# Optimization experiments

Measured on AMD Instinct MI355X. Metric: run time of the kernel, lower is better.

## Reference

```python
import jax, jax.numpy as jnp
import numpy as np
from jax import lax

Q = 8          # num quantization bins (co_matrix_shape[0])
K = 3          # spatial filter size (spatial_shape = [K,K,K])
PAD = (K - 1) // 2


def setup_inputs() -> dict:
    key = jax.random.key(0)
    k1, k2, k3 = jax.random.split(key, 3)
    # uniform [0,1) so floor((x-min)/max * Q) stays in [0, Q-1] (matches valid torch index_select)
    x = jax.random.uniform(k1, (8, 16, 256, 256), dtype=jnp.float32)
    co_matrix = jax.random.normal(k2, (Q, Q), dtype=jnp.float32)
    spatial_filter = jax.random.normal(k3, (K, K, K), dtype=jnp.float32)
    return {"input": x, "co_matrix": co_matrix, "spatial_filter": spatial_filter}


def _quantize(x, num_q):
    # faithful to the torch code: norm = (x - min) / max  (NOT max-min)
    x_min = jnp.min(x)
    x_max = jnp.max(x)
    idx = jnp.floor((x - x_min) / x_max * num_q).astype(jnp.int32)  # [N,c,h,w]
    return idx


def reference(input, co_matrix, spatial_filter):
    x = input
    N, c, h, w = x.shape
    idx = _quantize(x, Q)                                  # [N,c,h,w] int32

    # Vectorize the per-bin loop: gather row i of co_matrix at every pixel's bin index.
    # cof[i] = co_matrix[i, idx]  -> [Q,N,c,h,w]
    cof = co_matrix[:, idx]
    conv_in = (cof * x[None]).reshape(Q * N, 1, c, h, w)   # [Q*N,1,c,h,w]

    w3d = spatial_filter.reshape(1, 1, K, K, K)
    spatial = lax.conv_general_dilated(
        conv_in, w3d,
        window_strides=(1, 1, 1),
        padding=[(PAD, PAD)] * 3,
        dimension_numbers=("NCDHW", "OIDHW", "NCDHW"),
    ).reshape(Q, N, c, h, w)

    # torch code convolves the mask with a 1x1x1 ones filter at stride 1 -> identity
    mask = (idx[None] == jnp.arange(Q, dtype=jnp.int32)[:, None, None, None, None])
    conv_out = jnp.sum(mask.astype(x.dtype) * spatial, axis=0)  # [N,c,h,w]
    return (conv_out, co_matrix, spatial_filter, idx)
```

## Files before the change

kernel.cpp:

```cpp
#include <hip/hip_runtime.h>
#include <stdint.h>

typedef __fp16 h2 __attribute__((ext_vector_type(2)));

__device__ uint32_t g_slots[512];
__device__ __align__(16) uint32_t g_tbl[32];

__device__ __forceinline__ uint32_t mapf(float f) {
  uint32_t u = __float_as_uint(f);
  return (u & 0x80000000u) ? ~u : (u | 0x80000000u);
}
__device__ __forceinline__ float unmapf(uint32_t m) {
  return (m & 0x80000000u) ? __uint_as_float(m & 0x7FFFFFFFu) : __uint_as_float(~m);
}

__device__ __forceinline__ float fdot2f(h2 a, h2 b, float c) {
#if __has_builtin(__builtin_amdgcn_fdot2)
  return __builtin_amdgcn_fdot2(a, b, c, false);
#else
  float d;
  asm("v_dot2_f32_f16 %0, %1, %2, %3" : "=v"(d) : "v"(a), "v"(b), "v"(c));
  return d;
#endif
}

__global__ __launch_bounds__(256) void k_minmax(const float* __restrict__ x, int n4, int ntail,
                                                const float* __restrict__ co, const float* __restrict__ sfil,
                                                float* __restrict__ out_co, float* __restrict__ out_sf) {
  __shared__ float smn[256], smx[256];
  int tid = threadIdx.x;
  float mn = 3.0e38f, mx = -3.0e38f;
  const float4* x4 = (const float4*)x;
  int stride = gridDim.x * blockDim.x;
  #pragma unroll 4
  for (int i = blockIdx.x * blockDim.x + tid; i < n4; i += stride) {
    float4 v = x4[i];
    mn = fminf(mn, fminf(fminf(v.x, v.y), fminf(v.z, v.w)));
    mx = fmaxf(mx, fmaxf(fmaxf(v.x, v.y), fmaxf(v.z, v.w)));
  }
  if (blockIdx.x == 0 && tid == 0) {
    for (int i = 4 * n4; i < 4 * n4 + ntail; ++i) { mn = fminf(mn, x[i]); mx = fmaxf(mx, x[i]); }
  }
  smn[tid] = mn; smx[tid] = mx;
  __syncthreads();
  for (int s = 128; s > 0; s >>= 1) {
    if (tid < s) { smn[tid] = fminf(smn[tid], smn[tid + s]); smx[tid] = fmaxf(smx[tid], smx[tid + s]); }
    __syncthreads();
  }
  if (tid == 0) {
    int slot = (blockIdx.x & 15) * 16;
    atomicMax(&g_slots[slot], mapf(smx[0]));
    atomicMax(&g_slots[256 + slot], mapf(-smn[0]));
  }
  if (blockIdx.x == 0) {
    if (tid < 8) {
      const float* r = co + tid * 8;
      float rmn = r[0], rmx = r[0];
      #pragma unroll
      for (int j = 1; j < 8; ++j) { rmn = fminf(rmn, r[j]); rmx = fmaxf(rmx, r[j]); }
      float rs = (rmx - rmn) * (1.0f / 255.0f);
      if (rs < 1e-30f) rs = 1.0f;
      uint32_t d0 = 0, d1 = 0;
      #pragma unroll
      for (int j = 0; j < 8; ++j) {
        int b = (int)lrintf((r[j] - rmn) / rs);
        b = b < 0 ? 0 : (b > 255 ? 255 : b);
        if (j < 4) d0 |= ((uint32_t)b) << (8 * j);
        else       d1 |= ((uint32_t)b) << (8 * (j - 4));
      }
      g_tbl[4 * tid + 0] = d0;
      g_tbl[4 * tid + 1] = d1;
      g_tbl[4 * tid + 2] = __float_as_uint(rs);
      g_tbl[4 * tid + 3] = __float_as_uint(rmn);
    }
    if (tid < 64) out_co[tid] = co[tid];
    if (tid < 27) out_sf[tid] = sfil[tid];
  }
}

__device__ __forceinline__ float quant_d8(float xv, float mn, float mx8, float y8) {
  float s   = xv - mn;
  float t08 = s * y8;
  float r0  = __builtin_fmaf(-mx8, t08, s);
  return __builtin_fmaf(r0, y8, t08);
}

__global__ __launch_bounds__(256, 8) void k_conv(const float* __restrict__ x, const float* __restrict__ sfil,
                                              float* __restrict__ out, float* __restrict__ out_idx) {
  __shared__ __align__(16) uint32_t xsu[2640];
  __shared__ __align__(16) uint32_t qls[1320];
  __shared__ __align__(16) uint4    tbl[8];
  __shared__ uint32_t anyw[4];

  int tid = threadIdx.x;
  int b = blockIdx.x;
  int wt = b & 1, ht = (b >> 1) & 31, ct = (b >> 6) & 7, n = b >> 9;
  int c0 = ct * 2, h0 = ht * 8, w0 = wt * 128;
  int nbase = n * 16;

  if (tid < 8) tbl[tid] = ((const uint4*)g_tbl)[tid];

  uint32_t ma = 0u, mb = 0u;
  #pragma unroll
  for (int i = 0; i < 16; ++i) {
    uint32_t a = g_slots[i * 16], bq = g_slots[256 + i * 16];
    ma = ma > a ? ma : a;
    mb = mb > bq ? mb : bq;
  }
  float mx = unmapf(ma);
  float mn = -unmapf(mb);
  float y   = 1.0f / mx;
  float y8  = y * 8.0f;
  float mx8 = mx * 0.125f;

  const int tx = tid & 31, ty = tid >> 5;
  int qmaxv = 0;

  {
    #pragma unroll
    for (int it = 0; it < 5; ++it) {
      int rr = ty + 8 * it;
      int lc = (rr * 13) >> 7;
      int lh = rr - 10 * lc;
      int c = c0 - 1 + lc, h = h0 - 1 + lh;
      bool chok = ((unsigned)c < 16u) & ((unsigned)h < 256u);
      int chbase = ((nbase + c) << 16) + (h << 8);
      int wq = w0 + 4 * tx;
      float4 vb = float4{0.f, 0.f, 0.f, 0.f};
      if (chok) vb = *(const float4*)&x[chbase + wq];
      float pe = __shfl_up(vb.w, 1);
      if (tx == 0) {
        int wm = wq - 1;
        pe = (chok & (wm >= 0)) ? x[chbase + wm] : 0.0f;
      }
      float xv[4] = {pe, vb.x, vb.y, vb.z};
      uint32_t qu[4];
      #pragma unroll
      for (int j = 0; j < 4; ++j) {
        int q = (int)quant_d8(xv[j], mn, mx8, y8);
        qmaxv = max(qmaxv, q);
        qu[j] = min((uint32_t)q, 7u);
      }
      uint32_t b01 = __builtin_amdgcn_perm(qu[1], qu[0], 0x0c0c0400u);
      uint32_t b23 = __builtin_amdgcn_perm(qu[3], qu[2], 0x04000c0cu);
      h2 lo = __builtin_amdgcn_cvt_pkrtz(xv[0], xv[1]);
      h2 hi = __builtin_amdgcn_cvt_pkrtz(xv[2], xv[3]);
      uint2 wv; wv.x = __builtin_bit_cast(uint32_t, lo); wv.y = __builtin_bit_cast(uint32_t, hi);
      *(uint2*)&xsu[rr * 66 + 2 * tx] = wv;
      qls[rr * 33 + tx] = b01 | b23;
    }
    if (tid < 40) {
      int rr = tid;
      int lc = (rr * 13) >> 7;
      int lh = rr - 10 * lc;
      int c = c0 - 1 + lc, h = h0 - 1 + lh;
      bool chok = ((unsigned)c < 16u) & ((unsigned)h < 256u);
      int chbase = ((nbase + c) << 16) + (h << 8);
      int wq = w0 + 128;
      float4 vb = float4{0.f, 0.f, 0.f, 0.f};
      if (chok & (wq < 256)) vb = *(const float4*)&x[chbase + wq];
      float pe = chok ? x[chbase + wq - 1] : 0.0f;
      float xv[4] = {pe, vb.x, vb.y, vb.z};
      uint32_t qu[4];
      #pragma unroll
      for (int j = 0; j < 4; ++j) {
        int q = (int)quant_d8(xv[j], mn, mx8, y8);
        qmaxv = max(qmaxv, q);
        qu[j] = min((uint32_t)q, 7u);
      }
      uint32_t b01 = __builtin_amdgcn_perm(qu[1], qu[0], 0x0c0c0400u);
      uint32_t b23 = __builtin_amdgcn_perm(qu[3], qu[2], 0x04000c0cu);
      h2 lo = __builtin_amdgcn_cvt_pkrtz(xv[0], xv[1]);
      h2 hi = __builtin_amdgcn_cvt_pkrtz(xv[2], xv[3]);
      uint2 wv; wv.x = __builtin_bit_cast(uint32_t, lo); wv.y = __builtin_bit_cast(uint32_t, hi);
      *(uint2*)&xsu[rr * 66 + 64] = wv;
      qls[rr * 33 + 32] = b01 | b23;
    }
  }
  anyw[tid >> 6] = (uint32_t)__any(qmaxv > 7);
  __syncthreads();
  uint32_t any8 = anyw[0] | anyw[1] | anyw[2] | anyw[3];

  uint32_t wAs[9], wBs[9];
  #pragma unroll
  for (int r = 0; r < 9; ++r) {
    h2 a  = __builtin_amdgcn_cvt_pkrtz(sfil[3 * r], sfil[3 * r + 1]);
    h2 bq = __builtin_amdgcn_cvt_pkrtz(sfil[3 * r + 2], 0.0f);
    wAs[r] = (uint32_t)__builtin_amdgcn_readfirstlane((int)__builtin_bit_cast(uint32_t, a));
    wBs[r] = (uint32_t)__builtin_amdgcn_readfirstlane((int)__builtin_bit_cast(uint32_t, bq));
  }

  const h2 one2 = {(__fp16)1.0f, (__fp16)1.0f};
  const uint32_t SELK[4] = {0x03020100u, 0x04030201u, 0x05040302u, 0x06050403u};
  const int tw = tx, th = ty;

  for (int c = 0; c < 2; ++c) {
    int qbase = (c * 10 + th) * 33 + tw;
    int xbase = (c * 10 + th) * 66 + 2 * tw;

    int qc = qbase + 11 * 33;
    uint32_t Qc0 = qls[qc], Qc1 = qls[qc + 1];
    uint32_t q4 = __builtin_amdgcn_perm(Qc1, Qc0, 0x04030201u);
    uint32_t rlo[4], rhi[4]; float rs4[4], rcp4[4];
    #pragma unroll
    for (int k = 0; k < 4; ++k) {
      uint32_t qk = (q4 >> (8 * k)) & 0xffu;
      uint4 T = tbl[qk];
      rlo[k] = T.x; rhi[k] = T.y;
      rs4[k] = __uint_as_float(T.z);
      rcp4[k] = __builtin_fmaf(-1024.0f, rs4[k], __uint_as_float(T.w));
    }

    float acc1[4] = {0.f, 0.f, 0.f, 0.f};
    float acc2[4] = {0.f, 0.f, 0.f, 0.f};
    #pragma unroll
    for (int dc = 0; dc < 3; ++dc) {
      #pragma unroll
      for (int di = 0; di < 3; ++di) {
        int xo = xbase + (dc * 10 + di) * 66;
        int qo = qbase + (dc * 10 + di) * 33;
        uint2 px = *(const uint2*)&xsu[xo];
        uint32_t p2u = xsu[xo + 2];
        uint32_t Q0 = qls[qo], Q1 = qls[qo + 1];
        uint32_t m01 = __builtin_amdgcn_alignbit(px.y, px.x, 16);
        uint32_t m12 = __builtin_amdgcn_alignbit(p2u, px.y, 16);
        uint32_t xAu[4] = {px.x, m01, px.y, m12};
        uint32_t xBu[3] = {px.y, m12, p2u};
        int r = dc * 3 + di;
        h2 wA = __builtin_bit_cast(h2, wAs[r]);
        h2 wB = __builtin_bit_cast(h2, wBs[r]);
        h2 wB2 = __builtin_bit_cast(h2, wBs[r] << 16);
        #pragma unroll
        for (int k = 0; k < 4; ++k) {
          uint32_t sel = __builtin_amdgcn_perm(Q1, Q0, SELK[k]);
          uint32_t bb  = __builtin_amdgcn_perm(rhi[k], rlo[k], sel);
          uint32_t fA  = __builtin_amdgcn_perm(0x64646464u, bb, 0x04010400u);
          h2 pA = wA * __builtin_bit_cast(h2, xAu[k]);
          acc1[k] = fdot2f(pA, __builtin_bit_cast(h2, fA), acc1[k]);
          acc2[k] = fdot2f(pA, one2, acc2[k]);
          h2 pB; uint32_t fB;
          if (k < 3) {
            fB = __builtin_amdgcn_perm(0x64646464u, bb, 0x04040402u);
            pB = wB * __builtin_bit_cast(h2, xBu[k]);
          } else {
            fB = __builtin_amdgcn_perm(0x64646464u, bb, 0x04020404u);
            pB = wB2 * __builtin_bit_cast(h2, p2u);
          }
          acc1[k] = fdot2f(pB, __builtin_bit_cast(h2, fB), acc1[k]);
          acc2[k] = fdot2f(pB, one2, acc2[k]);
        }
      }
    }

    int gbase = ((nbase + c0 + c) << 16) + ((h0 + th) << 8) + (w0 + 4 * tw);
    float idxf[4], vals[4];
    if (!any8) {
      #pragma unroll
      for (int k = 0; k < 4; ++k) {
        idxf[k] = (float)((q4 >> (8 * k)) & 0xffu);
        vals[k] = __builtin_fmaf(rs4[k], acc1[k], rcp4[k] * acc2[k]);
      }
    } else {
      float4 cxv = *(const float4*)&x[gbase];
      float cx[4] = {cxv.x, cxv.y, cxv.z, cxv.w};
      #pragma unroll
      for (int k = 0; k < 4; ++k) {
        float d8 = quant_d8(cx[k], mn, mx8, y8);
        idxf[k] = truncf(d8);
        float v = __builtin_fmaf(rs4[k], acc1[k], rcp4[k] * acc2[k]);
        vals[k] = (d8 >= 8.0f) ? 0.0f : v;
      }
    }

    *(float4*)&out[gbase] = float4{vals[0], vals[1], vals[2], vals[3]};
    out_idx[gbase + 0] = idxf[0];
    *(float2*)&out_idx[gbase + 1] = float2{idxf[1], idxf[2]};
    out_idx[gbase + 3] = idxf[3];
  }
}

extern "C" void kernel_launch(void* const* d_in, const int* in_sizes, int n_in,
                              void* d_out, int out_size, void* d_ws, size_t ws_size,
                              hipStream_t stream) {
  const float* x    = (const float*)d_in[0];
  const float* co   = (const float*)d_in[1];
  const float* sfil = (const float*)d_in[2];
  float* out = (float*)d_out;
  int nx = in_sizes[0];

  int n4 = nx / 4, ntail = nx - 4 * n4;

  float* out_co  = out + nx;
  float* out_sf  = out + nx + 64;
  float* out_idx = out + nx + 64 + 27;

  k_minmax<<<512, 256, 0, stream>>>(x, n4, ntail, co, sfil, out_co, out_sf);
  k_conv<<<4096, 256, 0, stream>>>(x, sfil, out, out_idx);
}
```

Measured before the change: 124.5 us.

## Fuse min/max reduction and conv into one cooperative kernel with grid sync

Merges the global min/max reduction and the quantized 3D conv into a single cooperative kernel. A grid-wide barrier separates the two phases, and each block then processes two conv tiles. Each block builds the co-matrix table in shared memory itself instead of reading it from a global buffer. This removes a kernel launch and the gap between launches, at the cost of a grid sync and a residency requirement of 2048 blocks. If the cooperative launch fails, the code falls back to the two-kernel path.

Result: slower. 362.8 us (+191.5%).

```diff
diff --git a/kernel.cpp b/kernel.cpp
--- a/kernel.cpp
+++ b/kernel.cpp
@@ -1,5 +1,8 @@
 #include <hip/hip_runtime.h>
+#include <hip/hip_cooperative_groups.h>
 #include <stdint.h>
+
+namespace cg = cooperative_groups;
 
 typedef __fp16 h2 __attribute__((ext_vector_type(2)));
 
@@ -22,6 +25,267 @@
   asm("v_dot2_f32_f16 %0, %1, %2, %3" : "=v"(d) : "v"(a), "v"(b), "v"(c));
   return d;
 #endif
+}
+
+__device__ __forceinline__ float quant_d8(float xv, float mn, float mx8, float y8) {
+  float s   = xv - mn;
+  float t08 = s * y8;
+  float r0  = __builtin_fmaf(-mx8, t08, s);
+  return __builtin_fmaf(r0, y8, t08);
+}
+
+__device__ __forceinline__ uint4 build_tbl_row(const float* __restrict__ co, int row) {
+  const float* r = co + row * 8;
+  float rmn = r[0], rmx = r[0];
+  #pragma unroll
+  for (int j = 1; j < 8; ++j) { rmn = fminf(rmn, r[j]); rmx = fmaxf(rmx, r[j]); }
+  float rs = (rmx - rmn) * (1.0f / 255.0f);
+  if (rs < 1e-30f) rs = 1.0f;
+  uint32_t d0 = 0, d1 = 0;
+  #pragma unroll
+  for (int j = 0; j < 8; ++j) {
+    int b = (int)lrintf((r[j] - rmn) / rs);
+    b = b < 0 ? 0 : (b > 255 ? 255 : b);
+    if (j < 4) d0 |= ((uint32_t)b) << (8 * j);
+    else       d1 |= ((uint32_t)b) << (8 * (j - 4));
+  }
+  return uint4{d0, d1, __float_as_uint(rs), __float_as_uint(rmn)};
+}
+
+__global__ __launch_bounds__(256, 8) void k_fused(const float* __restrict__ x, int n4, int ntail,
+                                                  const float* __restrict__ co, const float* __restrict__ sfil,
+                                                  float* __restrict__ out, float* __restrict__ out_idx,
+                                                  float* __restrict__ out_co, float* __restrict__ out_sf) {
+  __shared__ __align__(16) uint32_t xsu[2640];
+  __shared__ __align__(16) uint32_t qls[1320];
+  __shared__ __align__(16) uint4    tbl[8];
+  __shared__ uint32_t anyw[4];
+
+  int tid = threadIdx.x;
+  int bid = blockIdx.x;
+
+  {
+    float* smn = (float*)xsu;
+    float* smx = smn + 256;
+    float mn = 3.0e38f, mx = -3.0e38f;
+    const float4* x4 = (const float4*)x;
+    int stride = gridDim.x * blockDim.x;
+    #pragma unroll 4
+    for (int i = bid * blockDim.x + tid; i < n4; i += stride) {
+      float4 v = x4[i];
+      mn = fminf(mn, fminf(fminf(v.x, v.y), fminf(v.z, v.w)));
+      mx = fmaxf(mx, fmaxf(fmaxf(v.x, v.y), fmaxf(v.z, v.w)));
+    }
+    if (bid == 0 && tid == 0) {
+      for (int i = 4 * n4; i < 4 * n4 + ntail; ++i) { mn = fminf(mn, x[i]); mx = fmaxf(mx, x[i]); }
+    }
+    smn[tid] = mn; smx[tid] = mx;
+    __syncthreads();
+    for (int s = 128; s > 0; s >>= 1) {
+      if (tid < s) { smn[tid] = fminf(smn[tid], smn[tid + s]); smx[tid] = fmaxf(smx[tid], smx[tid + s]); }
+      __syncthreads();
+    }
+    if (tid == 0) {
+      int slot = (bid & 15) * 16;
+      atomicMax(&g_slots[slot], mapf(smx[0]));
+      atomicMax(&g_slots[256 + slot], mapf(-smn[0]));
+    }
+    if (bid == 0) {
+      if (tid < 64) out_co[tid] = co[tid];
+      if (tid < 27) out_sf[tid] = sfil[tid];
+    }
+  }
+  __syncthreads();
+
+  if (tid < 8) tbl[tid] = build_tbl_row(co, tid);
+
+  cg::this_grid().sync();
+
+  uint32_t ma = 0u, mb = 0u;
+  #pragma unroll
+  for (int i = 0; i < 16; ++i) {
+    uint32_t a = g_slots[i * 16], bq = g_slots[256 + i * 16];
+    ma = ma > a ? ma : a;
+    mb = mb > bq ? mb : bq;
+  }
+  float mx = unmapf(ma);
+  float mn = -unmapf(mb);
+  float y   = 1.0f / mx;
+  float y8  = y * 8.0f;
+  float mx8 = mx * 0.125f;
+
+  uint32_t wAs[9], wBs[9];
+  #pragma unroll
+  for (int r = 0; r < 9; ++r) {
+    h2 a  = __builtin_amdgcn_cvt_pkrtz(sfil[3 * r], sfil[3 * r + 1]);
+    h2 bq = __builtin_amdgcn_cvt_pkrtz(sfil[3 * r + 2], 0.0f);
+    wAs[r] = (uint32_t)__builtin_amdgcn_readfirstlane((int)__builtin_bit_cast(uint32_t, a));
+    wBs[r] = (uint32_t)__builtin_amdgcn_readfirstlane((int)__builtin_bit_cast(uint32_t, bq));
+  }
+
+  const h2 one2 = {(__fp16)1.0f, (__fp16)1.0f};
+  const uint32_t SELK[4] = {0x03020100u, 0x04030201u, 0x05040302u, 0x06050403u};
+  const int tx = tid & 31, ty = tid >> 5;
+  const int tw = tx, th = ty;
+
+  for (int tt = 0; tt < 2; ++tt) {
+    int t = 2 * bid + tt;
+    int wt = t & 1, ht = (t >> 1) & 31, ct = (t >> 6) & 7, n = t >> 9;
+    int c0 = ct * 2, h0 = ht * 8, w0 = wt * 128;
+    int nbase = n * 16;
+    int qmaxv = 0;
+
+    __syncthreads();
+
+    {
+      #pragma unroll
+      for (int it = 0; it < 5; ++it) {
+        int rr = ty + 8 * it;
+        int lc = (rr * 13) >> 7;
+        int lh = rr - 10 * lc;
+        int c = c0 - 1 + lc, h = h0 - 1 + lh;
+        bool chok = ((unsigned)c < 16u) & ((unsigned)h < 256u);
+        int chbase = ((nbase + c) << 16) + (h << 8);
+        int wq = w0 + 4 * tx;
+        float4 vb = float4{0.f, 0.f, 0.f, 0.f};
+        if (chok) vb = *(const float4*)&x[chbase + wq];
+        float pe = __shfl_up(vb.w, 1);
+        if (tx == 0) {
+          int wm = wq - 1;
+          pe = (chok & (wm >= 0)) ? x[chbase + wm] : 0.0f;
+        }
+        float xv[4] = {pe, vb.x, vb.y, vb.z};
+        uint32_t qu[4];
+        #pragma unroll
+        for (int j = 0; j < 4; ++j) {
+          int q = (int)quant_d8(xv[j], mn, mx8, y8);
+          qmaxv = max(qmaxv, q);
+          qu[j] = min((uint32_t)q, 7u);
+        }
+        uint32_t b01 = __builtin_amdgcn_perm(qu[1], qu[0], 0x0c0c0400u);
+        uint32_t b23 = __builtin_amdgcn_perm(qu[3], qu[2], 0x04000c0cu);
+        h2 lo = __builtin_amdgcn_cvt_pkrtz(xv[0], xv[1]);
+        h2 hi = __builtin_amdgcn_cvt_pkrtz(xv[2], xv[3]);
+        uint2 wv; wv.x = __builtin_bit_cast(uint32_t, lo); wv.y = __builtin_bit_cast(uint32_t, hi);
+        *(uint2*)&xsu[rr * 66 + 2 * tx] = wv;
+        qls[rr * 33 + tx] = b01 | b23;
+      }
+      if (tid < 40) {
+        int rr = tid;
+        int lc = (rr * 13) >> 7;
+        int lh = rr - 10 * lc;
+        int c = c0 - 1 + lc, h = h0 - 1 + lh;
+        bool chok = ((unsigned)c < 16u) & ((unsigned)h < 256u);
+        int chbase = ((nbase + c) << 16) + (h << 8);
+        int wq = w0 + 128;
+        float4 vb = float4{0.f, 0.f, 0.f, 0.f};
+        if (chok & (wq < 256)) vb = *(const float4*)&x[chbase + wq];
+        float pe = chok ? x[chbase + wq - 1] : 0.0f;
+        float xv[4] = {pe, vb.x, vb.y, vb.z};
+        uint32_t qu[4];
+        #pragma unroll
+        for (int j = 0; j < 4; ++j) {
+          int q = (int)quant_d8(xv[j], mn, mx8, y8);
+          qmaxv = max(qmaxv, q);
+          qu[j] = min((uint32_t)q, 7u);
+        }
+        uint32_t b01 = __builtin_amdgcn_perm(qu[1], qu[0], 0x0c0c0400u);
+        uint32_t b23 = __builtin_amdgcn_perm(qu[3], qu[2], 0x04000c0cu);
+        h2 lo = __builtin_amdgcn_cvt_pkrtz(xv[0], xv[1]);
+        h2 hi = __builtin_amdgcn_cvt_pkrtz(xv[2], xv[3]);
+        uint2 wv; wv.x = __builtin_bit_cast(uint32_t, lo); wv.y = __builtin_bit_cast(uint32_t, hi);
+        *(uint2*)&xsu[rr * 66 + 64] = wv;
+        qls[rr * 33 + 32] = b01 | b23;
+      }
+    }
+    anyw[tid >> 6] = (uint32_t)__any(qmaxv > 7);
+    __syncthreads();
+    uint32_t any8 = anyw[0] | anyw[1] | anyw[2] | anyw[3];
+
+    for (int c = 0; c < 2; ++c) {
+      int qbase = (c * 10 + th) * 33 + tw;
+      int xbase = (c * 10 + th) * 66 + 2 * tw;
+
+      int qc = qbase + 11 * 33;
+      uint32_t Qc0 = qls[qc], Qc1 = qls[qc + 1];
+      uint32_t q4 = __builtin_amdgcn_perm(Qc1, Qc0, 0x04030201u);
+      uint32_t rlo[4], rhi[4]; float rs4[4], rcp4[4];
+      #pragma unroll
+      for (int k = 0; k < 4; ++k) {
+        uint32_t qk = (q4 >> (8 * k)) & 0xffu;
+        uint4 T = tbl[qk];
+        rlo[k] = T.x; rhi[k] = T.y;
+        rs4[k] = __uint_as_float(T.z);
+        rcp4[k] = __builtin_fmaf(-1024.0f, rs4[k], __uint_as_float(T.w));
+      }
+
+      float acc1[4] = {0.f, 0.f, 0.f, 0.f};
+      float acc2[4] = {0.f, 0.f, 0.f, 0.f};
+      #pragma unroll
+      for (int dc = 0; dc < 3; ++dc) {
+        #pragma unroll
+        for (int di = 0; di < 3; ++di) {
+          int xo = xbase + (dc * 10 + di) * 66;
+          int qo = qbase + (dc * 10 + di) * 33;
+          uint2 px = *(const uint2*)&xsu[xo];
+          uint32_t p2u = xsu[xo + 2];
+          uint32_t Q0 = qls[qo], Q1 = qls[qo + 1];
+          uint32_t m01 = __builtin_amdgcn_alignbit(px.y, px.x, 16);
+          uint32_t m12 = __builtin_amdgcn_alignbit(p2u, px.y, 16);
+          uint32_t xAu[4] = {px.x, m01, px.y, m12};
+          uint32_t xBu[3] = {px.y, m12, p2u};
+          int r = dc * 3 + di;
+          h2 wA = __builtin_bit_cast(h2, wAs[r]);
+          h2 wB = __builtin_bit_cast(h2, wBs[r]);
+          h2 wB2 = __builtin_bit_cast(h2, wBs[r] << 16);
+          #pragma unroll
+          for (int k = 0; k < 4; ++k) {
+            uint32_t sel = __builtin_amdgcn_perm(Q1, Q0, SELK[k]);
+            uint32_t bb  = __builtin_amdgcn_perm(rhi[k], rlo[k], sel);
+            uint32_t fA  = __builtin_amdgcn_perm(0x64646464u, bb, 0x04010400u);
+            h2 pA = wA * __builtin_bit_cast(h2, xAu[k]);
+            acc1[k] = fdot2f(pA, __builtin_bit_cast(h2, fA), acc1[k]);
+            acc2[k] = fdot2f(pA, one2, acc2[k]);
+            h2 pB; uint32_t fB;
+            if (k < 3) {
+              fB = __builtin_amdgcn_perm(0x64646464u, bb, 0x04040402u);
+              pB = wB * __builtin_bit_cast(h2, xBu[k]);
+            } else {
+              fB = __builtin_amdgcn_perm(0x64646464u, bb, 0x04020404u);
+              pB = wB2 * __builtin_bit_cast(h2, p2u);
+            }
+            acc1[k] = fdot2f(pB, __builtin_bit_cast(h2, fB), acc1[k]);
+            acc2[k] = fdot2f(pB, one2, acc2[k]);
+          }
+        }
+      }
+
+      int gbase = ((nbase + c0 + c) << 16) + ((h0 + th) << 8) + (w0 + 4 * tw);
+      float idxf[4], vals[4];
+      if (!any8) {
+        #pragma unroll
+        for (int k = 0; k < 4; ++k) {
+          idxf[k] = (float)((q4 >> (8 * k)) & 0xffu);
+          vals[k] = __builtin_fmaf(rs4[k], acc1[k], rcp4[k] * acc2[k]);
+        }
+      } else {
+        float4 cxv = *(const float4*)&x[gbase];
+        float cx[4] = {cxv.x, cxv.y, cxv.z, cxv.w};
+        #pragma unroll
+        for (int k = 0; k < 4; ++k) {
+          float d8 = quant_d8(cx[k], mn, mx8, y8);
+          idxf[k] = truncf(d8);
+          float v = __builtin_fmaf(rs4[k], acc1[k], rcp4[k] * acc2[k]);
+          vals[k] = (d8 >= 8.0f) ? 0.0f : v;
+        }
+      }
+
+      *(float4*)&out[gbase] = float4{vals[0], vals[1], vals[2], vals[3]};
+      out_idx[gbase + 0] = idxf[0];
+      *(float2*)&out_idx[gbase + 1] = float2{idxf[1], idxf[2]};
+      out_idx[gbase + 3] = idxf[3];
+    }
+  }
 }
 
 __global__ __launch_bounds__(256) void k_minmax(const float* __restrict__ x, int n4, int ntail,
@@ -54,35 +318,13 @@
   }
   if (blockIdx.x == 0) {
     if (tid < 8) {
-      const float* r = co + tid * 8;
-      float rmn = r[0], rmx = r[0];
-      #pragma unroll
-      for (int j = 1; j < 8; ++j) { rmn = fminf(rmn, r[j]); rmx = fmaxf(rmx, r[j]); }
-      float rs = (rmx - rmn) * (1.0f / 255.0f);
-      if (rs < 1e-30f) rs = 1.0f;
-      uint32_t d0 = 0, d1 = 0;
-      #pragma unroll
-      for (int j = 0; j < 8; ++j) {
-        int b = (int)lrintf((r[j] - rmn) / rs);
-        b = b < 0 ? 0 : (b > 255 ? 255 : b);
-        if (j < 4) d0 |= ((uint32_t)b) << (8 * j);
-        else       d1 |= ((uint32_t)b) << (8 * (j - 4));
-      }
-      g_tbl[4 * tid + 0] = d0;
-      g_tbl[4 * tid + 1] = d1;
-      g_tbl[4 * tid + 2] = __float_as_uint(rs);
-      g_tbl[4 * tid + 3] = __float_as_uint(rmn);
+      uint4 T = build_tbl_row(co, tid);
+      g_tbl[4 * tid + 0] = T.x; g_tbl[4 * tid + 1] = T.y;
+      g_tbl[4 * tid + 2] = T.z; g_tbl[4 * tid + 3] = T.w;
     }
     if (tid < 64) out_co[tid] = co[tid];
     if (tid < 27) out_sf[tid] = sfil[tid];
   }
-}
-
-__device__ __forceinline__ float quant_d8(float xv, float mn, float mx8, float y8) {
-  float s   = xv - mn;
-  float t08 = s * y8;
-  float r0  = __builtin_fmaf(-mx8, t08, s);
-  return __builtin_fmaf(r0, y8, t08);
 }
 
 __global__ __launch_bounds__(256, 8) void k_conv(const float* __restrict__ x, const float* __restrict__ sfil,
@@ -294,6 +536,12 @@
   float* out_sf  = out + nx + 64;
   float* out_idx = out + nx + 64 + 27;
 
-  k_minmax<<<512, 256, 0, stream>>>(x, n4, ntail, co, sfil, out_co, out_sf);
-  k_conv<<<4096, 256, 0, stream>>>(x, sfil, out, out_idx);
-}
+  void* args[] = {(void*)&x, (void*)&n4, (void*)&ntail, (void*)&co, (void*)&sfil,
+                  (void*)&out, (void*)&out_idx, (void*)&out_co, (void*)&out_sf};
+  hipError_t e = hipLaunchCooperativeKernel((const void*)k_fused, dim3(2048), dim3(256),
+                                            args, 0, stream);
+  if (e != hipSuccess) {
+    k_minmax<<<512, 256, 0, stream>>>(x, n4, ntail, co, sfil, out_co, out_sf);
+    k_conv<<<4096, 256, 0, stream>>>(x, sfil, out, out_idx);
+  }
+}
```

## Share LDS plane loads across two output channels in the 3D stencil loop

Applied to the files above, without the earlier changes.

Restructures the per-thread loop so both output channels are accumulated together. Each input depth plane is loaded from LDS once and reused for every output channel whose 3-tap window covers it, so 12 row loads serve both channels instead of 18. The byte-select perms are also computed once per row rather than once per channel. In exchange it keeps two sets of accumulators and table entries live, which raises register pressure and may lower occupancy.

Result: slower. 205.0 us (+64.7%).

```diff
diff --git a/kernel.cpp b/kernel.cpp
--- a/kernel.cpp
+++ b/kernel.cpp
@@ -194,50 +194,57 @@
   const uint32_t SELK[4] = {0x03020100u, 0x04030201u, 0x05040302u, 0x06050403u};
   const int tw = tx, th = ty;
 
+  uint32_t q4c[2];
+  uint32_t rlo[2][4], rhi[2][4];
+  #pragma unroll
   for (int c = 0; c < 2; ++c) {
-    int qbase = (c * 10 + th) * 33 + tw;
-    int xbase = (c * 10 + th) * 66 + 2 * tw;
-
-    int qc = qbase + 11 * 33;
+    int qc = (c * 10 + th) * 33 + tw + 11 * 33;
     uint32_t Qc0 = qls[qc], Qc1 = qls[qc + 1];
     uint32_t q4 = __builtin_amdgcn_perm(Qc1, Qc0, 0x04030201u);
-    uint32_t rlo[4], rhi[4]; float rs4[4], rcp4[4];
+    q4c[c] = q4;
     #pragma unroll
     for (int k = 0; k < 4; ++k) {
       uint32_t qk = (q4 >> (8 * k)) & 0xffu;
       uint4 T = tbl[qk];
-      rlo[k] = T.x; rhi[k] = T.y;
-      rs4[k] = __uint_as_float(T.z);
-      rcp4[k] = __builtin_fmaf(-1024.0f, rs4[k], __uint_as_float(T.w));
-    }
-
-    float acc1[4] = {0.f, 0.f, 0.f, 0.f};
-    float acc2[4] = {0.f, 0.f, 0.f, 0.f};
+      rlo[c][k] = T.x; rhi[c][k] = T.y;
+    }
+  }
+
+  float acc1[2][4] = {{0.f,0.f,0.f,0.f},{0.f,0.f,0.f,0.f}};
+  float acc2[2][4] = {{0.f,0.f,0.f,0.f},{0.f,0.f,0.f,0.f}};
+
+  #pragma unroll
+  for (int a = 0; a < 4; ++a) {
     #pragma unroll
-    for (int dc = 0; dc < 3; ++dc) {
-      #pragma unroll
-      for (int di = 0; di < 3; ++di) {
-        int xo = xbase + (dc * 10 + di) * 66;
-        int qo = qbase + (dc * 10 + di) * 33;
-        uint2 px = *(const uint2*)&xsu[xo];
-        uint32_t p2u = xsu[xo + 2];
-        uint32_t Q0 = qls[qo], Q1 = qls[qo + 1];
-        uint32_t m01 = __builtin_amdgcn_alignbit(px.y, px.x, 16);
-        uint32_t m12 = __builtin_amdgcn_alignbit(p2u, px.y, 16);
-        uint32_t xAu[4] = {px.x, m01, px.y, m12};
-        uint32_t xBu[3] = {px.y, m12, p2u};
+    for (int di = 0; di < 3; ++di) {
+      int row = a * 10 + th + di;
+      int xo = row * 66 + 2 * tw;
+      int qo = row * 33 + tw;
+      uint2 px = *(const uint2*)&xsu[xo];
+      uint32_t p2u = xsu[xo + 2];
+      uint32_t Q0 = qls[qo], Q1 = qls[qo + 1];
+      uint32_t m01 = __builtin_amdgcn_alignbit(px.y, px.x, 16);
+      uint32_t m12 = __builtin_amdgcn_alignbit(p2u, px.y, 16);
+      uint32_t xAu[4] = {px.x, m01, px.y, m12};
+      uint32_t xBu[3] = {px.y, m12, p2u};
+      uint32_t sel[4];
+      #pragma unroll
+      for (int k = 0; k < 4; ++k) sel[k] = __builtin_amdgcn_perm(Q1, Q0, SELK[k]);
+      #pragma unroll
+      for (int c = 0; c < 2; ++c) {
+        int dc = a - c;
+        if (dc < 0 || dc > 2) continue;
         int r = dc * 3 + di;
         h2 wA = __builtin_bit_cast(h2, wAs[r]);
         h2 wB = __builtin_bit_cast(h2, wBs[r]);
         h2 wB2 = __builtin_bit_cast(h2, wBs[r] << 16);
         #pragma unroll
         for (int k = 0; k < 4; ++k) {
-          uint32_t sel = __builtin_amdgcn_perm(Q1, Q0, SELK[k]);
-          uint32_t bb  = __builtin_amdgcn_perm(rhi[k], rlo[k], sel);
-          uint32_t fA  = __builtin_amdgcn_perm(0x64646464u, bb, 0x04010400u);
+          uint32_t bb = __builtin_amdgcn_perm(rhi[c][k], rlo[c][k], sel[k]);
+          uint32_t fA = __builtin_amdgcn_perm(0x64646464u, bb, 0x04010400u);
           h2 pA = wA * __builtin_bit_cast(h2, xAu[k]);
-          acc1[k] = fdot2f(pA, __builtin_bit_cast(h2, fA), acc1[k]);
-          acc2[k] = fdot2f(pA, one2, acc2[k]);
+          acc1[c][k] = fdot2f(pA, __builtin_bit_cast(h2, fA), acc1[c][k]);
+          acc2[c][k] = fdot2f(pA, one2, acc2[c][k]);
           h2 pB; uint32_t fB;
           if (k < 3) {
             fB = __builtin_amdgcn_perm(0x64646464u, bb, 0x04040402u);
@@ -246,10 +253,23 @@
             fB = __builtin_amdgcn_perm(0x64646464u, bb, 0x04020404u);
             pB = wB2 * __builtin_bit_cast(h2, p2u);
           }
-          acc1[k] = fdot2f(pB, __builtin_bit_cast(h2, fB), acc1[k]);
-          acc2[k] = fdot2f(pB, one2, acc2[k]);
+          acc1[c][k] = fdot2f(pB, __builtin_bit_cast(h2, fB), acc1[c][k]);
+          acc2[c][k] = fdot2f(pB, one2, acc2[c][k]);
         }
       }
+    }
+  }
+
+  #pragma unroll
+  for (int c = 0; c < 2; ++c) {
+    uint32_t q4 = q4c[c];
+    float rs4[4], rcp4[4];
+    #pragma unroll
+    for (int k = 0; k < 4; ++k) {
+      uint32_t qk = (q4 >> (8 * k)) & 0xffu;
+      uint4 T = tbl[qk];
+      rs4[k] = __uint_as_float(T.z);
+      rcp4[k] = __builtin_fmaf(-1024.0f, rs4[k], __uint_as_float(T.w));
     }
 
     int gbase = ((nbase + c0 + c) << 16) + ((h0 + th) << 8) + (w0 + 4 * tw);
@@ -258,7 +278,7 @@
       #pragma unroll
       for (int k = 0; k < 4; ++k) {
         idxf[k] = (float)((q4 >> (8 * k)) & 0xffu);
-        vals[k] = __builtin_fmaf(rs4[k], acc1[k], rcp4[k] * acc2[k]);
+        vals[k] = __builtin_fmaf(rs4[k], acc1[c][k], rcp4[k] * acc2[c][k]);
       }
     } else {
       float4 cxv = *(const float4*)&x[gbase];
@@ -267,7 +287,7 @@
       for (int k = 0; k < 4; ++k) {
         float d8 = quant_d8(cx[k], mn, mx8, y8);
         idxf[k] = truncf(d8);
-        float v = __builtin_fmaf(rs4[k], acc1[k], rcp4[k] * acc2[k]);
+        float v = __builtin_fmaf(rs4[k], acc1[c][k], rcp4[k] * acc2[c][k]);
         vals[k] = (d8 >= 8.0f) ? 0.0f : v;
       }
     }
```
